# Optimization experiments

Hardware: AMD Instinct MI355X
Metric: run time of the kernel (lower is better)

The kernel has to match this reference:

```python
import jax, jax.numpy as jnp
import numpy as np

EPS = 1e-05
RMS_EPS = 1e-06


def activation_quant(x, num_bits=8):
    # per-token (last-dim) abs-max int8 fake quant, computed in fp32
    qn = -(2 ** (num_bits - 1))
    qp = 2 ** (num_bits - 1) - 1
    xf = x.astype(jnp.float32)
    s = qp / jnp.clip(jnp.max(jnp.abs(xf), axis=-1, keepdims=True), EPS, None)
    return (jnp.clip(jnp.round(xf * s), qn, qp) / s).astype(x.dtype)


def weight_quant(w):
    # full-tensor abs-mean ternary fake quant
    wf = w.astype(jnp.float32)
    s = 1.0 / jnp.clip(jnp.mean(jnp.abs(wf)), EPS, None)
    return (jnp.clip(jnp.round(wf * s), -1.0, 1.0) / s).astype(w.dtype)


def bit_linear(x, w):
    # STE wrappers (identity in forward value, straight-through in grad)
    qx = x + jax.lax.stop_gradient(activation_quant(x) - x)
    qw = w + jax.lax.stop_gradient(weight_quant(w) - w)
    return jnp.einsum('bsh,oh->bso', qx, qw)


def rms_norm(x, weight, eps=RMS_EPS):
    xf = x.astype(jnp.float32)
    var = jnp.mean(xf * xf, axis=-1, keepdims=True)
    return weight * (xf * jax.lax.rsqrt(var + eps)).astype(x.dtype)


def setup_inputs() -> dict:
    key = jax.random.key(0)
    k1, k2, k3, k4 = jax.random.split(key, 4)
    B, S, H, I = 2, 2048, 2048, 8192
    scale = 1.0 / np.sqrt(H)
    return {
        'x': jax.random.normal(k1, (B, S, H), dtype=jnp.float32),
        'w_gate': jax.random.normal(k2, (I, H), dtype=jnp.float32) * scale,
        'w_up': jax.random.normal(k3, (I, H), dtype=jnp.float32) * scale,
        'w_down': jax.random.normal(k4, (H, I), dtype=jnp.float32) * (1.0 / np.sqrt(I)),
        'ln_weight': jnp.ones((I,), dtype=jnp.float32),
    }


def reference(x, w_gate, w_up, w_down, ln_weight):
    h = jax.nn.silu(bit_linear(x, w_gate)) * bit_linear(x, w_up)
    h = rms_norm(h, ln_weight)
    return bit_linear(h, w_down)
```

## Files before the change

### kernel.cpp

```cpp
#include <hip/hip_runtime.h>
#include <stdint.h>

typedef int v4i __attribute__((ext_vector_type(4)));

#define TOKENS 4096
#define HDIM   2048
#define IDIM   8192
#define WN     16777216
#define NBLK   512
#define BANDP  5e-7f

#define MFMA_I8 __builtin_amdgcn_mfma_i32_16x16x64_i8

static __device__ __forceinline__ void gload_lds16(const void* g, void* l) {
  __builtin_amdgcn_global_load_lds(
      (const __attribute__((address_space(1))) void*)(unsigned long long)(uintptr_t)g,
      (__attribute__((address_space(3))) void*)(unsigned)(uintptr_t)l,
      16, 0, 0);
}

static __device__ __forceinline__ double wsum64d(double v) {
#pragma unroll
  for (int m = 32; m; m >>= 1) v += __shfl_xor(v, m, 64);
  return v;
}
static __device__ __forceinline__ double wmax64d(double v) {
#pragma unroll
  for (int m = 32; m; m >>= 1) v = fmax(v, __shfl_xor(v, m, 64));
  return v;
}
static __device__ __forceinline__ float wmax64f(float v) {
#pragma unroll
  for (int m = 32; m; m >>= 1) v = fmaxf(v, __shfl_xor(v, m, 64));
  return v;
}

static __device__ __forceinline__ int q8f(float v, float s, float lo, float hi) {
  float p = v * s;
  return (int)fminf(fmaxf(rintf(p), lo), hi);
}
static __device__ __forceinline__ uint32_t packq_f(float4 v, float s) {
  int a = q8f(v.x, s, -128.f, 127.f);
  int b = q8f(v.y, s, -128.f, 127.f);
  int c = q8f(v.z, s, -128.f, 127.f);
  int d = q8f(v.w, s, -128.f, 127.f);
  return (uint32_t)((a & 255) | ((b & 255) << 8) | ((c & 255) << 16) | ((d & 255) << 24));
}

__global__ __launch_bounds__(256) void wsum_leaf(const float* __restrict__ wg,
                                                 const float* __restrict__ wu,
                                                 const float* __restrict__ wd,
                                                 float* __restrict__ part) {
  const float* w = blockIdx.y == 0 ? wg : (blockIdx.y == 1 ? wu : wd);
  int tid = threadIdx.x;
  int wv = tid >> 6, lane = tid & 63;
  int lf = lane >> 1, m = lane & 1;
  __shared__ float A[256], B[256];
  const float4* w4 = (const float4*)w;
#pragma unroll
  for (int p = 0; p < 2; ++p) {
    int leaf = wv * 64 + p * 32 + lf;
    size_t b4 = ((size_t)blockIdx.x * 256 + leaf) * 32;
    float4 v = w4[b4 + m];
    float r0 = fabsf(v.x), r1 = fabsf(v.y), r2 = fabsf(v.z), r3 = fabsf(v.w);
    for (int k = 1; k < 16; ++k) {
      float4 u = w4[b4 + m + 2 * k];
      r0 += fabsf(u.x); r1 += fabsf(u.y); r2 += fabsf(u.z); r3 += fabsf(u.w);
    }
    float s = (r0 + r1) + (r2 + r3);
    float o = __shfl_xor(s, 1, 64);
    if (m == 0) A[leaf] = s + o;
  }
  __syncthreads();
  float* src = A; float* dst = B;
  for (int n = 128; n >= 1; n >>= 1) {
    if (tid < n) dst[tid] = src[2 * tid] + src[2 * tid + 1];
    __syncthreads();
    float* t = src; src = dst; dst = t;
  }
  if (tid == 0) part[blockIdx.y * NBLK + blockIdx.x] = src[0];
}

__global__ __launch_bounds__(256) void wsum_final(const float* __restrict__ part,
                                                  float* __restrict__ wsc) {
  int t = blockIdx.x, tid = threadIdx.x;
  __shared__ float A[512], B[256];
  A[tid] = part[t * NBLK + tid];
  A[tid + 256] = part[t * NBLK + tid + 256];
  __syncthreads();
  float* src = A; float* dst = B;
  for (int n = 256; n >= 1; n >>= 1) {
    if (tid < n) dst[tid] = src[2 * tid] + src[2 * tid + 1];
    __syncthreads();
    float* tmp = src; src = dst; dst = tmp;
  }
  if (tid == 0) {
    float mean32 = src[0] / (float)WN;
    float m32 = fmaxf(mean32, 1e-5f);
    float s32 = 1.0f / m32;
    wsc[t] = s32;
    wsc[3 + t] = 1.0f / s32;
  }
}

__global__ __launch_bounds__(256) void wquant_kernel(const float* __restrict__ wg,
                                                     const float* __restrict__ wu,
                                                     const float* __restrict__ wd,
                                                     const float* __restrict__ wsc,
                                                     int8_t* __restrict__ qg,
                                                     int8_t* __restrict__ qu,
                                                     int8_t* __restrict__ qd) {
  int t = blockIdx.y;
  const float* w = t == 0 ? wg : (t == 1 ? wu : wd);
  int8_t* q = t == 0 ? qg : (t == 1 ? qu : qd);
  float s32 = wsc[t];
  const float4* w4 = (const float4*)w;
  uint32_t* q4 = (uint32_t*)q;
  const int n4 = WN / 4;
  for (int i = blockIdx.x * 256 + threadIdx.x; i < n4; i += gridDim.x * 256) {
    float4 v = w4[i];
    float vv[4] = {v.x, v.y, v.z, v.w};
    int o[4];
#pragma unroll
    for (int j = 0; j < 4; ++j) {
      float pf = fabsf(vv[j]) * s32;
      int q2 = 2 * (int)fminf(rintf(pf), 1.0f);
      if (fabsf(pf - 0.5f) < BANDP) q2 = 1;
      o[j] = (vv[j] < 0.0f) ? -q2 : q2;
    }
    q4[i] = (uint32_t)((o[0] & 255) | ((o[1] & 255) << 8) |
                       ((o[2] & 255) << 16) | ((o[3] & 255) << 24));
  }
}

__global__ __launch_bounds__(256) void xquant_kernel(const float* __restrict__ x,
                                                     int8_t* __restrict__ qx,
                                                     double* __restrict__ axd) {
  int row = blockIdx.x, tid = threadIdx.x;
  const float4* xr = (const float4*)(x + (size_t)row * HDIM);
  float4 v0 = xr[tid], v1 = xr[tid + 256];
  float m = fmaxf(fmaxf(fmaxf(fabsf(v0.x), fabsf(v0.y)), fmaxf(fabsf(v0.z), fabsf(v0.w))),
                  fmaxf(fmaxf(fabsf(v1.x), fabsf(v1.y)), fmaxf(fabsf(v1.z), fabsf(v1.w))));
  m = wmax64f(m);
  __shared__ float red[4];
  int wid = tid >> 6, lane = tid & 63;
  if (lane == 0) red[wid] = m;
  __syncthreads();
  float mm = fmaxf(fmaxf(red[0], red[1]), fmaxf(red[2], red[3]));
  float c32 = fmaxf(mm, 1e-5f);
  float s32 = 127.0f / c32;
  if (tid == 0) axd[row] = 1.0 / (double)s32;
  uint32_t* q4 = (uint32_t*)(qx + (size_t)row * HDIM);
  q4[tid] = packq_f(v0, s32);
  q4[tid + 256] = packq_f(v1, s32);
}

__global__ __launch_bounds__(512, 4) void gemm1_kernel(const int8_t* __restrict__ qx,
                                                       const int8_t* __restrict__ qg,
                                                       const int8_t* __restrict__ qu,
                                                       const float* __restrict__ wsc,
                                                       const double* __restrict__ axd,
                                                       float* __restrict__ h) {
  extern __shared__ char lds[];
  int tid = threadIdx.x, wid = tid >> 6, lane = tid & 63;
  int l15 = lane & 15, lgp = lane >> 4;
  int wr = wid >> 2, wc = wid & 3;
  int flat = blockIdx.y * 64 + blockIdx.x;
  int xcd = flat & 7, local = flat >> 3;
  int mt = local >> 3, nl = local & 7;
  int m0 = mt * 128, n0 = (xcd * 8 + nl) * 128;
  const int8_t* bA = qx + (size_t)m0 * HDIM;
  const int8_t* bG = qg + (size_t)n0 * HDIM;
  const int8_t* bU = qu + (size_t)n0 * HDIM;

  v4i accg[4][2], accu[4][2];
  v4i vzero = {0, 0, 0, 0};
#pragma unroll
  for (int i = 0; i < 4; ++i)
#pragma unroll
    for (int j = 0; j < 2; ++j) { accg[i][j] = vzero; accu[i][j] = vzero; }

  int aoff[4], goff[2], uoff[2];
#pragma unroll
  for (int i = 0; i < 4; ++i)
    aoff[i] = lgp * 2048 + (wr * 64 + i * 16 + l15) * 16;
#pragma unroll
  for (int i = 0; i < 2; ++i) {
    goff[i] = 8192 + lgp * 2048 + (wc * 32 + i * 16 + l15) * 16;
    uoff[i] = goff[i] + 8192;
  }

  int srow = tid & 127, sslab = tid >> 7;
  const size_t rA = (size_t)srow * HDIM;
  int sdst = sslab * 2048 + srow * 16;

  const int NT = HDIM / 64;
  {
    size_t k0 = (size_t)sslab * 16;
    gload_lds16(bA + rA + k0, lds + sdst);
    gload_lds16(bG + rA + k0, lds + sdst + 8192);
    gload_lds16(bU + rA + k0, lds + sdst + 16384);
    size_t k1 = 64 + (size_t)sslab * 16;
    gload_lds16(bA + rA + k1, lds + 24576 + sdst);
    gload_lds16(bG + rA + k1, lds + 24576 + sdst + 8192);
    gload_lds16(bU + rA + k1, lds + 24576 + sdst + 16384);
  }
  asm volatile("s_waitcnt vmcnt(3)" ::: "memory");
  __builtin_amdgcn_s_barrier();
  __builtin_amdgcn_sched_barrier(0);

  int c0 = 0, c1 = 24576, c2 = 49152;
  for (int t = 0; t < NT; ++t) {
    const bool pf = (t + 2 < NT);
    size_t koff = (size_t)(t + 2) * 64 + sslab * 16;
    v4i a0 = *(const v4i*)(lds + c0 + aoff[0]);
    v4i a1 = *(const v4i*)(lds + c0 + aoff[1]);
    v4i a2 = *(const v4i*)(lds + c0 + aoff[2]);
    v4i a3 = *(const v4i*)(lds + c0 + aoff[3]);
    v4i bg0 = *(const v4i*)(lds + c0 + goff[0]);
    v4i bg1 = *(const v4i*)(lds + c0 + goff[1]);
    if (pf) {
      gload_lds16(bA + rA + koff, lds + c2 + sdst);
      gload_lds16(bG + rA + koff, lds + c2 + sdst + 8192);
    }
    __builtin_amdgcn_s_barrier();
    asm volatile("s_waitcnt lgkmcnt(0)" ::: "memory");
    __builtin_amdgcn_sched_barrier(0);
    __builtin_amdgcn_s_setprio(1);
    accg[0][0] = MFMA_I8(a0, bg0, accg[0][0], 0, 0, 0);
    accg[0][1] = MFMA_I8(a0, bg1, accg[0][1], 0, 0, 0);
    accg[1][0] = MFMA_I8(a1, bg0, accg[1][0], 0, 0, 0);
    accg[1][1] = MFMA_I8(a1, bg1, accg[1][1], 0, 0, 0);
    accg[2][0] = MFMA_I8(a2, bg0, accg[2][0], 0, 0, 0);
    accg[2][1] = MFMA_I8(a2, bg1, accg[2][1], 0, 0, 0);
    accg[3][0] = MFMA_I8(a3, bg0, accg[3][0], 0, 0, 0);
    accg[3][1] = MFMA_I8(a3, bg1, accg[3][1], 0, 0, 0);
    __builtin_amdgcn_s_setprio(0);
    __builtin_amdgcn_s_barrier();
    v4i bu0 = *(const v4i*)(lds + c0 + uoff[0]);
    v4i bu1 = *(const v4i*)(lds + c0 + uoff[1]);
    if (pf) gload_lds16(bU + rA + koff, lds + c2 + sdst + 16384);
    if (pf)
      asm volatile("s_waitcnt vmcnt(3)" ::: "memory");
    else
      asm volatile("s_waitcnt vmcnt(0)" ::: "memory");
    __builtin_amdgcn_s_barrier();
    asm volatile("s_waitcnt lgkmcnt(0)" ::: "memory");
    __builtin_amdgcn_sched_barrier(0);
    __builtin_amdgcn_s_setprio(1);
    accu[0][0] = MFMA_I8(a0, bu0, accu[0][0], 0, 0, 0);
    accu[0][1] = MFMA_I8(a0, bu1, accu[0][1], 0, 0, 0);
    accu[1][0] = MFMA_I8(a1, bu0, accu[1][0], 0, 0, 0);
    accu[1][1] = MFMA_I8(a1, bu1, accu[1][1], 0, 0, 0);
    accu[2][0] = MFMA_I8(a2, bu0, accu[2][0], 0, 0, 0);
    accu[2][1] = MFMA_I8(a2, bu1, accu[2][1], 0, 0, 0);
    accu[3][0] = MFMA_I8(a3, bu0, accu[3][0], 0, 0, 0);
    accu[3][1] = MFMA_I8(a3, bu1, accu[3][1], 0, 0, 0);
    __builtin_amdgcn_s_setprio(0);
    __builtin_amdgcn_s_barrier();
    int tmp = c0; c0 = c1; c1 = c2; c2 = tmp;
  }

  double mg = 0.5 * (double)wsc[3 + 0];
  double mu = 0.5 * (double)wsc[3 + 1];
#pragma unroll
  for (int mi = 0; mi < 4; ++mi) {
#pragma unroll
    for (int rg = 0; rg < 4; ++rg) {
      int grow = m0 + wr * 64 + mi * 16 + lgp * 4 + rg;
      double axr = axd[grow];
      double sg = axr * mg, su = axr * mu;
#pragma unroll
      for (int ni = 0; ni < 2; ++ni) {
        int gcol = n0 + wc * 32 + ni * 16 + l15;
        double g = (double)accg[mi][ni][rg] * sg;
        double u = (double)accu[mi][ni][rg] * su;
        double sig = 1.0 / (1.0 + exp(-g));
        h[(size_t)grow * IDIM + gcol] = (float)((g * sig) * u);
      }
    }
  }
}

__global__ __launch_bounds__(256) void hquant_kernel(const float* __restrict__ h,
                                                     const float* __restrict__ lnw,
                                                     double* __restrict__ ahd,
                                                     int8_t* __restrict__ qh) {
  int row = blockIdx.x, tid = threadIdx.x;
  const float4* hr = (const float4*)(h + (size_t)row * IDIM);
  const float4* lw4 = (const float4*)lnw;
  float4 hv[8], wv[8];
  double ssq = 0.0;
#pragma unroll
  for (int i = 0; i < 8; ++i) {
    hv[i] = hr[tid + i * 256];
    wv[i] = lw4[tid + i * 256];
    ssq += (double)hv[i].x * hv[i].x + (double)hv[i].y * hv[i].y +
           (double)hv[i].z * hv[i].z + (double)hv[i].w * hv[i].w;
  }
  ssq = wsum64d(ssq);
  __shared__ double redd[4];
  __shared__ double redm[4];
  int wid = tid >> 6, lane = tid & 63;
  if (lane == 0) redd[wid] = ssq;
  __syncthreads();
  double tot = redd[0] + redd[1] + redd[2] + redd[3];
  double rd = 1.0 / sqrt(tot * (1.0 / (double)IDIM) + 1e-6);
  double mx = 0.0;
#pragma unroll
  for (int i = 0; i < 8; ++i) {
    double y0 = (double)wv[i].x * ((double)hv[i].x * rd);
    double y1 = (double)wv[i].y * ((double)hv[i].y * rd);
    double y2 = (double)wv[i].z * ((double)hv[i].z * rd);
    double y3 = (double)wv[i].w * ((double)hv[i].w * rd);
    mx = fmax(mx, fmax(fmax(fabs(y0), fabs(y1)), fmax(fabs(y2), fabs(y3))));
  }
  mx = wmax64d(mx);
  if (lane == 0) redm[wid] = mx;
  __syncthreads();
  double mm = fmax(fmax(redm[0], redm[1]), fmax(redm[2], redm[3]));
  float c32 = fmaxf((float)mm, 1e-5f);
  float s32 = 127.0f / c32;
  double sd = (double)s32;
  if (tid == 0) ahd[row] = 1.0 / (double)s32;
  uint32_t* q4 = (uint32_t*)(qh + (size_t)row * IDIM);
#pragma unroll
  for (int i = 0; i < 8; ++i) {
    double y0 = (double)wv[i].x * ((double)hv[i].x * rd);
    double y1 = (double)wv[i].y * ((double)hv[i].y * rd);
    double y2 = (double)wv[i].z * ((double)hv[i].z * rd);
    double y3 = (double)wv[i].w * ((double)hv[i].w * rd);
    int a = (int)fmin(fmax(rint(y0 * sd), -128.0), 127.0);
    int b = (int)fmin(fmax(rint(y1 * sd), -128.0), 127.0);
    int c = (int)fmin(fmax(rint(y2 * sd), -128.0), 127.0);
    int d = (int)fmin(fmax(rint(y3 * sd), -128.0), 127.0);
    q4[tid + i * 256] = (uint32_t)((a & 255) | ((b & 255) << 8) | ((c & 255) << 16) | ((d & 255) << 24));
  }
}

__global__ __launch_bounds__(512, 4) void gemm2_kernel(const int8_t* __restrict__ qh,
                                                       const int8_t* __restrict__ qd,
                                                       const float* __restrict__ wsc,
                                                       const double* __restrict__ ahd,
                                                       float* __restrict__ out) {
  extern __shared__ char lds[];
  int tid = threadIdx.x, wid = tid >> 6, lane = tid & 63;
  int l15 = lane & 15, lgp = lane >> 4;
  int wr = wid >> 2, wc = wid & 3;
  int flat = blockIdx.y * 16 + blockIdx.x;
  int xcd = flat & 7, local = flat >> 3;
  int mt = xcd * 4 + (local >> 4), nt = local & 15;
  int m0 = mt * 128, n0 = nt * 128;
  const int8_t* bA = qh + (size_t)m0 * IDIM;
  const int8_t* bB = qd + (size_t)n0 * IDIM;

  v4i acc[4][2];
  v4i vzero = {0, 0, 0, 0};
#pragma unroll
  for (int i = 0; i < 4; ++i)
#pragma unroll
    for (int j = 0; j < 2; ++j) acc[i][j] = vzero;

  int aoff[4], boff[2];
#pragma unroll
  for (int i = 0; i < 4; ++i)
    aoff[i] = lgp * 2048 + (wr * 64 + i * 16 + l15) * 16;
#pragma unroll
  for (int i = 0; i < 2; ++i)
    boff[i] = 8192 + lgp * 2048 + (wc * 32 + i * 16 + l15) * 16;

  int srow = tid & 127, sslab = tid >> 7;
  const size_t rA = (size_t)srow * IDIM;
  int sdst = sslab * 2048 + srow * 16;

  const int NT = IDIM / 64;
  {
    size_t k0 = (size_t)sslab * 16;
    gload_lds16(bA + rA + k0, lds + sdst);
    gload_lds16(bB + rA + k0, lds + sdst + 8192);
    size_t k1 = 64 + (size_t)sslab * 16;
    gload_lds16(bA + rA + k1, lds + 16384 + sdst);
    gload_lds16(bB + rA + k1, lds + 16384 + sdst + 8192);
  }
  asm volatile("s_waitcnt vmcnt(2)" ::: "memory");
  __builtin_amdgcn_s_barrier();
  __builtin_amdgcn_sched_barrier(0);

  int c0 = 0, c1 = 16384, c2 = 32768;
  for (int t = 0; t < NT; ++t) {
    const bool pf = (t + 2 < NT);
    size_t koff = (size_t)(t + 2) * 64 + sslab * 16;
    v4i a0 = *(const v4i*)(lds + c0 + aoff[0]);
    v4i a1 = *(const v4i*)(lds + c0 + aoff[1]);
    v4i b0 = *(const v4i*)(lds + c0 + boff[0]);
    v4i b1 = *(const v4i*)(lds + c0 + boff[1]);
    if (pf) gload_lds16(bA + rA + koff, lds + c2 + sdst);
    __builtin_amdgcn_s_barrier();
    asm volatile("s_waitcnt lgkmcnt(0)" ::: "memory");
    __builtin_amdgcn_sched_barrier(0);
    __builtin_amdgcn_s_setprio(1);
    acc[0][0] = MFMA_I8(a0, b0, acc[0][0], 0, 0, 0);
    acc[0][1] = MFMA_I8(a0, b1, acc[0][1], 0, 0, 0);
    acc[1][0] = MFMA_I8(a1, b0, acc[1][0], 0, 0, 0);
    acc[1][1] = MFMA_I8(a1, b1, acc[1][1], 0, 0, 0);
    __builtin_amdgcn_s_setprio(0);
    __builtin_amdgcn_s_barrier();
    v4i a2 = *(const v4i*)(lds + c0 + aoff[2]);
    v4i a3 = *(const v4i*)(lds + c0 + aoff[3]);
    if (pf) gload_lds16(bB + rA + koff, lds + c2 + sdst + 8192);
    if (pf)
      asm volatile("s_waitcnt vmcnt(2)" ::: "memory");
    else
      asm volatile("s_waitcnt vmcnt(0)" ::: "memory");
    __builtin_amdgcn_s_barrier();
    asm volatile("s_waitcnt lgkmcnt(0)" ::: "memory");
    __builtin_amdgcn_sched_barrier(0);
    __builtin_amdgcn_s_setprio(1);
    acc[2][0] = MFMA_I8(a2, b0, acc[2][0], 0, 0, 0);
    acc[2][1] = MFMA_I8(a2, b1, acc[2][1], 0, 0, 0);
    acc[3][0] = MFMA_I8(a3, b0, acc[3][0], 0, 0, 0);
    acc[3][1] = MFMA_I8(a3, b1, acc[3][1], 0, 0, 0);
    __builtin_amdgcn_s_setprio(0);
    __builtin_amdgcn_s_barrier();
    int tmp = c0; c0 = c1; c1 = c2; c2 = tmp;
  }

  double md = 0.5 * (double)wsc[3 + 2];
#pragma unroll
  for (int mi = 0; mi < 4; ++mi) {
#pragma unroll
    for (int rg = 0; rg < 4; ++rg) {
      int grow = m0 + wr * 64 + mi * 16 + lgp * 4 + rg;
      double sc = ahd[grow] * md;
#pragma unroll
      for (int ni = 0; ni < 2; ++ni) {
        int gcol = n0 + wc * 32 + ni * 16 + l15;
        out[(size_t)grow * HDIM + gcol] = (float)((double)acc[mi][ni][rg] * sc);
      }
    }
  }
}

extern "C" void kernel_launch(void* const* d_in, const int* in_sizes, int n_in,
                              void* d_out, int out_size, void* d_ws, size_t ws_size,
                              hipStream_t stream) {
  const float* x   = (const float*)d_in[0];
  const float* wg  = (const float*)d_in[1];
  const float* wu  = (const float*)d_in[2];
  const float* wd  = (const float*)d_in[3];
  const float* lnw = (const float*)d_in[4];
  float* out = (float*)d_out;
  char* ws = (char*)d_ws;

  size_t off = 0;
  auto alloc = [&](size_t b) { size_t o = off; off += (b + 255) & ~(size_t)255; return o; };
  size_t o_wsc  = alloc(8 * 4);
  size_t o_part = alloc(3 * NBLK * 4);
  size_t o_axd  = alloc((size_t)TOKENS * 8);
  size_t o_ahd  = alloc((size_t)TOKENS * 8);
  size_t o_qx   = alloc((size_t)TOKENS * HDIM);
  size_t o_qg   = alloc((size_t)IDIM * HDIM);
  size_t o_qu   = alloc((size_t)IDIM * HDIM);
  size_t o_qd   = alloc((size_t)HDIM * IDIM);
  size_t o_h    = alloc((size_t)TOKENS * IDIM * 4);
  (void)ws_size; (void)in_sizes; (void)n_in; (void)out_size; (void)o_qu;

  float* wsc  = (float*)(ws + o_wsc);
  float* part = (float*)(ws + o_part);
  double* axd = (double*)(ws + o_axd);
  double* ahd = (double*)(ws + o_ahd);
  int8_t* qx  = (int8_t*)(ws + o_qx);
  int8_t* qg  = (int8_t*)(ws + o_qg);
  int8_t* qu  = (int8_t*)(ws + o_qu);
  int8_t* qd  = (int8_t*)(ws + o_qd);
  int8_t* qh  = (int8_t*)(ws + o_qg);
  float* h    = (float*)(ws + o_h);

  wsum_leaf<<<dim3(NBLK, 3), 256, 0, stream>>>(wg, wu, wd, part);
  wsum_final<<<3, 256, 0, stream>>>(part, wsc);
  wquant_kernel<<<dim3(1024, 3), 256, 0, stream>>>(wg, wu, wd, wsc, qg, qu, qd);
  xquant_kernel<<<TOKENS, 256, 0, stream>>>(x, qx, axd);
  gemm1_kernel<<<dim3(IDIM / 128, TOKENS / 128), 512, 3 * 24576, stream>>>(qx, qg, qu, wsc, axd, h);
  hquant_kernel<<<TOKENS, 256, 0, stream>>>(h, lnw, ahd, qh);
  gemm2_kernel<<<dim3(HDIM / 128, TOKENS / 128), 512, 3 * 16384, stream>>>(qh, qd, wsc, ahd, out);
}
```

Measured before the change: 501.2 us.

## Double gemm1 M-tile to 256 rows to raise weight reuse per block

The gate/up int8 GEMM now computes a 256x128 output tile per block instead of 128x128. Each wave holds eight A fragments, so every B fragment loaded into LDS is reused across twice as many rows, and the grid halves. The triple-buffered LDS grows to 96 KB, held in static shared memory, with prefetch loads split across four MFMA phases. In exchange, accumulator register pressure doubles, launch bounds drop to 2 blocks per CU, and fewer blocks may hurt load balance.

Measured after the change: 461.1 us. -8.0%, faster.

```diff
diff --git a/kernel.cpp b/kernel.cpp
--- a/kernel.cpp
+++ b/kernel.cpp
@@ -155,64 +155,67 @@
   q4[tid + 256] = packq_f(v1, s32);
 }
 
-__global__ __launch_bounds__(512, 4) void gemm1_kernel(const int8_t* __restrict__ qx,
+__global__ __launch_bounds__(512, 2) void gemm1_kernel(const int8_t* __restrict__ qx,
                                                        const int8_t* __restrict__ qg,
                                                        const int8_t* __restrict__ qu,
                                                        const float* __restrict__ wsc,
                                                        const double* __restrict__ axd,
                                                        float* __restrict__ h) {
-  extern __shared__ char lds[];
+  __shared__ char lds[98304];
   int tid = threadIdx.x, wid = tid >> 6, lane = tid & 63;
   int l15 = lane & 15, lgp = lane >> 4;
   int wr = wid >> 2, wc = wid & 3;
   int flat = blockIdx.y * 64 + blockIdx.x;
   int xcd = flat & 7, local = flat >> 3;
   int mt = local >> 3, nl = local & 7;
-  int m0 = mt * 128, n0 = (xcd * 8 + nl) * 128;
+  int m0 = mt * 256, n0 = (xcd * 8 + nl) * 128;
   const int8_t* bA = qx + (size_t)m0 * HDIM;
   const int8_t* bG = qg + (size_t)n0 * HDIM;
   const int8_t* bU = qu + (size_t)n0 * HDIM;
 
-  v4i accg[4][2], accu[4][2];
+  v4i accg[8][2], accu[8][2];
   v4i vzero = {0, 0, 0, 0};
 #pragma unroll
-  for (int i = 0; i < 4; ++i)
+  for (int i = 0; i < 8; ++i)
 #pragma unroll
     for (int j = 0; j < 2; ++j) { accg[i][j] = vzero; accu[i][j] = vzero; }
 
-  int aoff[4], goff[2], uoff[2];
-#pragma unroll
-  for (int i = 0; i < 4; ++i)
-    aoff[i] = lgp * 2048 + (wr * 64 + i * 16 + l15) * 16;
+  int aoff[8], goff[2], uoff[2];
+#pragma unroll
+  for (int i = 0; i < 8; ++i)
+    aoff[i] = lgp * 4096 + (wr * 128 + i * 16 + l15) * 16;
 #pragma unroll
   for (int i = 0; i < 2; ++i) {
-    goff[i] = 8192 + lgp * 2048 + (wc * 32 + i * 16 + l15) * 16;
+    goff[i] = 16384 + lgp * 2048 + (wc * 32 + i * 16 + l15) * 16;
     uoff[i] = goff[i] + 8192;
   }
 
-  int srow = tid & 127, sslab = tid >> 7;
-  const size_t rA = (size_t)srow * HDIM;
-  int sdst = sslab * 2048 + srow * 16;
+  int rA8 = tid & 255, sA = tid >> 8;
+  int sdA0 = sA * 4096 + rA8 * 16;
+  int sdA1 = sdA0 + 8192;
+  const size_t gA = (size_t)rA8 * HDIM;
+  int rG = tid & 127, sG = tid >> 7;
+  int sdG = 16384 + sG * 2048 + rG * 16;
+  const size_t gG = (size_t)rG * HDIM;
 
   const int NT = HDIM / 64;
-  {
-    size_t k0 = (size_t)sslab * 16;
-    gload_lds16(bA + rA + k0, lds + sdst);
-    gload_lds16(bG + rA + k0, lds + sdst + 8192);
-    gload_lds16(bU + rA + k0, lds + sdst + 16384);
-    size_t k1 = 64 + (size_t)sslab * 16;
-    gload_lds16(bA + rA + k1, lds + 24576 + sdst);
-    gload_lds16(bG + rA + k1, lds + 24576 + sdst + 8192);
-    gload_lds16(bU + rA + k1, lds + 24576 + sdst + 16384);
-  }
-  asm volatile("s_waitcnt vmcnt(3)" ::: "memory");
+#pragma unroll
+  for (int t0 = 0; t0 < 2; ++t0) {
+    int cb = t0 * 32768;
+    size_t kt = (size_t)t0 * 64;
+    gload_lds16(bA + gA + kt + sA * 16,        lds + cb + sdA0);
+    gload_lds16(bA + gA + kt + 32 + sA * 16,   lds + cb + sdA1);
+    gload_lds16(bG + gG + kt + sG * 16,        lds + cb + sdG);
+    gload_lds16(bU + gG + kt + sG * 16,        lds + cb + sdG + 8192);
+  }
+  asm volatile("s_waitcnt vmcnt(4)" ::: "memory");
   __builtin_amdgcn_s_barrier();
   __builtin_amdgcn_sched_barrier(0);
 
-  int c0 = 0, c1 = 24576, c2 = 49152;
+  int c0 = 0, c1 = 32768, c2 = 65536;
   for (int t = 0; t < NT; ++t) {
     const bool pf = (t + 2 < NT);
-    size_t koff = (size_t)(t + 2) * 64 + sslab * 16;
+    size_t kt2 = (size_t)(t + 2) * 64;
     v4i a0 = *(const v4i*)(lds + c0 + aoff[0]);
     v4i a1 = *(const v4i*)(lds + c0 + aoff[1]);
     v4i a2 = *(const v4i*)(lds + c0 + aoff[2]);
@@ -220,8 +223,8 @@
     v4i bg0 = *(const v4i*)(lds + c0 + goff[0]);
     v4i bg1 = *(const v4i*)(lds + c0 + goff[1]);
     if (pf) {
-      gload_lds16(bA + rA + koff, lds + c2 + sdst);
-      gload_lds16(bG + rA + koff, lds + c2 + sdst + 8192);
+      gload_lds16(bA + gA + kt2 + sA * 16,      lds + c2 + sdA0);
+      gload_lds16(bA + gA + kt2 + 32 + sA * 16, lds + c2 + sdA1);
     }
     __builtin_amdgcn_s_barrier();
     asm volatile("s_waitcnt lgkmcnt(0)" ::: "memory");
@@ -237,13 +240,28 @@
     accg[3][1] = MFMA_I8(a3, bg1, accg[3][1], 0, 0, 0);
     __builtin_amdgcn_s_setprio(0);
     __builtin_amdgcn_s_barrier();
+    v4i a4 = *(const v4i*)(lds + c0 + aoff[4]);
+    v4i a5 = *(const v4i*)(lds + c0 + aoff[5]);
+    v4i a6 = *(const v4i*)(lds + c0 + aoff[6]);
+    v4i a7 = *(const v4i*)(lds + c0 + aoff[7]);
+    if (pf) gload_lds16(bG + gG + kt2 + sG * 16, lds + c2 + sdG);
+    __builtin_amdgcn_s_barrier();
+    asm volatile("s_waitcnt lgkmcnt(0)" ::: "memory");
+    __builtin_amdgcn_sched_barrier(0);
+    __builtin_amdgcn_s_setprio(1);
+    accg[4][0] = MFMA_I8(a4, bg0, accg[4][0], 0, 0, 0);
+    accg[4][1] = MFMA_I8(a4, bg1, accg[4][1], 0, 0, 0);
+    accg[5][0] = MFMA_I8(a5, bg0, accg[5][0], 0, 0, 0);
+    accg[5][1] = MFMA_I8(a5, bg1, accg[5][1], 0, 0, 0);
+    accg[6][0] = MFMA_I8(a6, bg0, accg[6][0], 0, 0, 0);
+    accg[6][1] = MFMA_I8(a6, bg1, accg[6][1], 0, 0, 0);
+    accg[7][0] = MFMA_I8(a7, bg0, accg[7][0], 0, 0, 0);
+    accg[7][1] = MFMA_I8(a7, bg1, accg[7][1], 0, 0, 0);
+    __builtin_amdgcn_s_setprio(0);
+    __builtin_amdgcn_s_barrier();
     v4i bu0 = *(const v4i*)(lds + c0 + uoff[0]);
     v4i bu1 = *(const v4i*)(lds + c0 + uoff[1]);
-    if (pf) gload_lds16(bU + rA + koff, lds + c2 + sdst + 16384);
-    if (pf)
-      asm volatile("s_waitcnt vmcnt(3)" ::: "memory");
-    else
-      asm volatile("s_waitcnt vmcnt(0)" ::: "memory");
+    if (pf) gload_lds16(bU + gG + kt2 + sG * 16, lds + c2 + sdG + 8192);
     __builtin_amdgcn_s_barrier();
     asm volatile("s_waitcnt lgkmcnt(0)" ::: "memory");
     __builtin_amdgcn_sched_barrier(0);
@@ -258,16 +276,33 @@
     accu[3][1] = MFMA_I8(a3, bu1, accu[3][1], 0, 0, 0);
     __builtin_amdgcn_s_setprio(0);
     __builtin_amdgcn_s_barrier();
+    if (pf)
+      asm volatile("s_waitcnt vmcnt(4)" ::: "memory");
+    else
+      asm volatile("s_waitcnt vmcnt(0)" ::: "memory");
+    __builtin_amdgcn_s_barrier();
+    __builtin_amdgcn_sched_barrier(0);
+    __builtin_amdgcn_s_setprio(1);
+    accu[4][0] = MFMA_I8(a4, bu0, accu[4][0], 0, 0, 0);
+    accu[4][1] = MFMA_I8(a4, bu1, accu[4][1], 0, 0, 0);
+    accu[5][0] = MFMA_I8(a5, bu0, accu[5][0], 0, 0, 0);
+    accu[5][1] = MFMA_I8(a5, bu1, accu[5][1], 0, 0, 0);
+    accu[6][0] = MFMA_I8(a6, bu0, accu[6][0], 0, 0, 0);
+    accu[6][1] = MFMA_I8(a6, bu1, accu[6][1], 0, 0, 0);
+    accu[7][0] = MFMA_I8(a7, bu0, accu[7][0], 0, 0, 0);
+    accu[7][1] = MFMA_I8(a7, bu1, accu[7][1], 0, 0, 0);
+    __builtin_amdgcn_s_setprio(0);
+    __builtin_amdgcn_s_barrier();
     int tmp = c0; c0 = c1; c1 = c2; c2 = tmp;
   }
 
   double mg = 0.5 * (double)wsc[3 + 0];
   double mu = 0.5 * (double)wsc[3 + 1];
 #pragma unroll
-  for (int mi = 0; mi < 4; ++mi) {
+  for (int mi = 0; mi < 8; ++mi) {
 #pragma unroll
     for (int rg = 0; rg < 4; ++rg) {
-      int grow = m0 + wr * 64 + mi * 16 + lgp * 4 + rg;
+      int grow = m0 + wr * 128 + mi * 16 + lgp * 4 + rg;
       double axr = axd[grow];
       double sg = axr * mg, su = axr * mu;
 #pragma unroll
@@ -480,7 +515,7 @@
   wsum_final<<<3, 256, 0, stream>>>(part, wsc);
   wquant_kernel<<<dim3(1024, 3), 256, 0, stream>>>(wg, wu, wd, wsc, qg, qu, qd);
   xquant_kernel<<<TOKENS, 256, 0, stream>>>(x, qx, axd);
-  gemm1_kernel<<<dim3(IDIM / 128, TOKENS / 128), 512, 3 * 24576, stream>>>(qx, qg, qu, wsc, axd, h);
+  gemm1_kernel<<<dim3(IDIM / 128, TOKENS / 256), 512, 0, stream>>>(qx, qg, qu, wsc, axd, h);
   hquant_kernel<<<TOKENS, 256, 0, stream>>>(h, lnw, ahd, qh);
   gemm2_kernel<<<dim3(HDIM / 128, TOKENS / 128), 512, 3 * 16384, stream>>>(qh, qd, wsc, ahd, out);
 }
```
